# Kernel tuning notes

Measured on AMD Instinct MI355X. Metric: run time of the kernel, lower is better.

## Reference

```python
import jax, jax.numpy as jnp
import numpy as np
from jax import lax

E = 16          # num_experts
CAP = 256       # capacity
MAX_IT = 3      # max_iterations
LPF = 2.0       # load_penalty_factor
DTEMP = 2.0     # diversity_temp
MIN_USAGE = 0.05
NC = 10         # num_classes
TC = 256        # trunk_channels
B = 2048
MIN_TOK = max(1, int(B * MIN_USAGE))        # 102
K_STATIC = min(B, max(CAP, MIN_TOK))        # static top-k width per expert claim


def setup_inputs() -> dict:
    key = jax.random.key(0)
    ks = jax.random.split(key, 16)
    d = {}
    d['x'] = jax.random.normal(ks[0], (B, 3, 32, 32), jnp.float32)
    chans = [(3, 32), (32, 64), (64, 128), (128, 256)]
    for i, (ci, co) in enumerate(chans, 1):
        d[f'cw{i}'] = jax.random.normal(ks[i], (co, ci, 3, 3), jnp.float32) * (1.0 / np.sqrt(ci * 9))
        d[f'cb{i}'] = jnp.zeros((co,), jnp.float32)
        d[f'g{i}'] = jnp.ones((co,), jnp.float32)
        d[f'be{i}'] = jnp.zeros((co,), jnp.float32)
        d[f'm{i}'] = jnp.zeros((co,), jnp.float32)
        d[f'v{i}'] = jnp.ones((co,), jnp.float32)
    d['gw1'] = jax.random.normal(ks[5], (E, TC, TC // 2), jnp.float32) * 0.05
    d['gb1'] = jnp.zeros((E, TC // 2), jnp.float32)
    d['gw2'] = jax.random.normal(ks[6], (E, TC // 2), jnp.float32) * 0.05
    d['gb2'] = jnp.zeros((E,), jnp.float32)
    d['cls_w'] = jax.random.normal(ks[7], (E, NC, TC), jnp.float32) * 0.01
    d['cls_b'] = jnp.zeros((E, NC), jnp.float32)
    d['usage_ema'] = jnp.ones((E,), jnp.float32) / E
    return d


def _conv_bn_relu(x, w, b, g, beta, m, v):
    y = lax.conv_general_dilated(x, w, (1, 1), 'SAME', dimension_numbers=('NCHW', 'OIHW', 'NCHW'))
    y = y + b[None, :, None, None]
    scale = (g / jnp.sqrt(v + 1e-5))[None, :, None, None]
    return jax.nn.relu((y - m[None, :, None, None]) * scale + beta[None, :, None, None])


def _maxpool2(x):
    return lax.reduce_window(x, -jnp.inf, lax.max, (1, 1, 2, 2), (1, 1, 2, 2), 'VALID')


def _forward(x, cw1, cb1, g1, be1, m1, v1, cw2, cb2, g2, be2, m2, v2,
             cw3, cb3, g3, be3, m3, v3, cw4, cb4, g4, be4, m4, v4,
             gw1, gb1, gw2, gb2, cls_w, cls_b, usage_ema):
    # trunk (eval-mode BN)
    h = _conv_bn_relu(x, cw1, cb1, g1, be1, m1, v1)
    h = _conv_bn_relu(h, cw2, cb2, g2, be2, m2, v2)
    h = _maxpool2(h)
    h = _conv_bn_relu(h, cw3, cb3, g3, be3, m3, v3)
    h = _conv_bn_relu(h, cw4, cb4, g4, be4, m4, v4)
    h = _maxpool2(h)
    feats = h.mean(axis=(2, 3))  # AdaptiveAvgPool2d(1)+Flatten -> [B, TC]

    # per-expert classifier heads
    logits_e = jnp.einsum('bd,ecd->bec', feats, cls_w) + cls_b[None]  # [B,E,NC]
    probs = jax.nn.softmax(logits_e, axis=2)
    ent = -(probs * jnp.log(jnp.clip(probs, 1e-12))).sum(axis=2)      # [B,E]
    confidence = -ent

    # per-expert gates (vectorized over experts); dropout is identity in eval
    hidden = jax.nn.relu(jnp.einsum('bd,edh->beh', feats, gw1) + gb1[None])
    expert_scores = (jnp.einsum('beh,eh->be', hidden, gw2) + gb2[None]) / DTEMP

    routing_scores = 0.6 * expert_scores + 0.4 * confidence - LPF * usage_ema[None]

    # iterative capacity-constrained routing (eval: expert order 0..E-1)
    D = jnp.zeros((B, E), bool)
    loads = jnp.zeros((E,), jnp.float32)
    avail = jnp.ones((B,), bool)
    ranks = jnp.arange(K_STATIC)
    for it in range(MAX_IT):
        # penalty from loads at the START of the iteration
        pscores = routing_scores - (it + 1) * LPF * loads[None]
        for j in range(E):
            sj = jnp.where(avail, pscores[:, j], -jnp.inf)
            vc = avail.sum().astype(jnp.int32)
            rc = jnp.maximum(0, CAP - loads[j].astype(jnp.int32))
            ntc = jnp.where((rc == 0) | (vc == 0), 0,
                            jnp.maximum(jnp.minimum(rc, vc), jnp.minimum(MIN_TOK, vc)))
            _, idx = lax.top_k(sj, K_STATIC)
            take = ranks < ntc
            claimed = jnp.zeros((B,), bool).at[idx].set(take)
            D = D.at[:, j].set(D[:, j] | claimed)
            avail = avail & ~claimed
            loads = loads.at[j].add(ntc.astype(jnp.float32))

    # fallback: sequentially assign leftover tokens to least-loaded of top-3
    def fb(carry, inp):
        Dc, lc = carry
        sc, av, i = inp
        _, t3 = lax.top_k(sc, 3)
        best = t3[jnp.argmin(lc[t3])]
        Dc = Dc.at[i, best].set(Dc[i, best] | av)
        lc = lc.at[best].add(av.astype(jnp.float32))
        return (Dc, lc), None

    (D, loads), _ = lax.scan(fb, (D, loads), (routing_scores, avail, jnp.arange(B)))

    Df = D.astype(jnp.float32)
    active = routing_scores * Df
    active = active - active.max(axis=1, keepdims=True)
    weights = jax.nn.softmax(active + (Df - 1.0) * 1e9, axis=1)
    final_logits = (weights[:, :, None] * logits_e).sum(axis=1)
    return final_logits, routing_scores, D


def reference(x, cw1, cb1, g1, be1, m1, v1, cw2, cb2, g2, be2, m2, v2,
              cw3, cb3, g3, be3, m3, v3, cw4, cb4, g4, be4, m4, v4,
              gw1, gb1, gw2, gb2, cls_w, cls_b, usage_ema):
    return _forward(x, cw1, cb1, g1, be1, m1, v1, cw2, cb2, g2, be2, m2, v2,
                    cw3, cb3, g3, be3, m3, v3, cw4, cb4, g4, be4, m4, v4,
                    gw1, gb1, gw2, gb2, cls_w, cls_b, usage_ema)
```

## Files before the change

### kernel.cpp

```cpp
#include <hip/hip_runtime.h>

typedef __attribute__((ext_vector_type(8))) short short8;
typedef __attribute__((ext_vector_type(4))) float f32x4;

__device__ __forceinline__ unsigned short f2bf(float f) {
  unsigned u = __float_as_uint(f);
  unsigned r = (u + 0x7fffu + ((u >> 16) & 1u)) >> 16;
  return (unsigned short)r;
}
__device__ __forceinline__ float bf2f(unsigned short h) {
  return __uint_as_float(((unsigned)h) << 16);
}

__global__ __launch_bounds__(256) void bnprep_kernel(
    const float* __restrict__ g, const float* __restrict__ be,
    const float* __restrict__ m, const float* __restrict__ v,
    const float* __restrict__ b, float* __restrict__ A, float* __restrict__ C, int n)
{
  int i = blockIdx.x * 256 + threadIdx.x;
  if (i < n) {
    float s = g[i] / sqrtf(v[i] + 1e-5f);
    A[i] = s;
    C[i] = (b[i] - m[i]) * s + be[i];
  }
}

__global__ __launch_bounds__(256) void wprep2_kernel(
    const float* __restrict__ w, unsigned short* __restrict__ wPk, int CO, int CI)
{
  int NCB = CI / 32, NF = CO / 16;
  int total = 9 * NCB * NF * 64;
  int idx = blockIdx.x * 256 + threadIdx.x;
  if (idx >= total) return;
  int lane = idx & 63;
  int unit = idx >> 6;
  int f = unit % NF;
  int cb = (unit / NF) % NCB;
  int s = unit / (NF * NCB);
  int co = f * 16 + (lane & 15);
  int ci0 = cb * 32 + (lane >> 4) * 8;
  long base = (long)unit * 1024 + lane * 8;
  #pragma unroll
  for (int j = 0; j < 8; ++j) {
    float v = w[((long)co * CI + ci0 + j) * 9 + s];
    unsigned short h = f2bf(v);
    unsigned short l = f2bf(v - bf2f(h));
    wPk[base + j] = h;
    wPk[base + 512 + j] = l;
  }
}

__global__ __launch_bounds__(512, 2) void conv12_kernel(
    const float* __restrict__ xin, const float* __restrict__ cw1,
    const float* __restrict__ A1p, const float* __restrict__ C1p,
    const unsigned short* __restrict__ wPk, const float* __restrict__ Ap,
    const float* __restrict__ Cp, unsigned short* __restrict__ outA)
{
  constexpr int TY = 16, TX = 32;
  constexpr int PXW = TX + 2;
  constexpr int PXT = (TY + 2) * PXW;
  constexpr int PLSTR = PXT * 8 + 8;
  constexpr int NF = 4;
  __shared__ alignas(16) unsigned short smem[8 * PLSTR];
  __shared__ alignas(16) float sx[2160];
  __shared__ alignas(16) float sw[864];

  const int nwg = gridDim.x;
  const int orig = blockIdx.x;
  const int q = nwg >> 3, r = nwg & 7;
  const int xcd = orig & 7, pos = orig >> 3;
  const int bx = (xcd < r ? xcd * (q + 1) : r * (q + 1) + (xcd - r) * q) + pos;

  const int img = bx >> 1;
  const int tY0 = (bx & 1) * 16;

  const int tid = threadIdx.x;
  const int lane = tid & 63;
  const int lx = lane & 15, kg = lane >> 4;
  const int w = tid >> 6;

  for (int i = tid; i < 2160; i += 512) {
    int c = i / 720, rem = i - c * 720;
    int yy = rem / 36, xx2 = rem - yy * 36;
    int gy = tY0 + yy - 2, gx = xx2 - 2;
    sx[i] = (gy >= 0 && gy < 32 && gx >= 0 && gx < 32)
            ? xin[(long)img * 3072 + c * 1024 + gy * 32 + gx] : 0.f;
  }
  for (int i = tid; i < 864; i += 512) {
    int co = i & 31, kk = i >> 5;
    sw[kk * 32 + co] = cw1[(long)co * 27 + kk];
  }
  __syncthreads();

  #pragma unroll 1
  for (int p = 0; p < 2; ++p) {
    int px = p * 512 + tid;
    if (px < PXT) {
      int ry = px / PXW, rx = px - ry * PXW;
      int gy = tY0 + ry - 1, gx = rx - 1;
      if (gy >= 0 && gy < 32 && gx >= 0 && gx < 32) {
        #pragma unroll 1
        for (int half = 0; half < 2; ++half) {
          float acc[16];
          #pragma unroll
          for (int j = 0; j < 16; ++j) acc[j] = 0.f;
          #pragma unroll
          for (int c = 0; c < 3; ++c) {
            #pragma unroll
            for (int k = 0; k < 9; ++k) {
              int dy = k / 3, dx = k - 3 * (k / 3);
              float iv = sx[c * 720 + (ry + dy) * 36 + rx + dx];
              const float4* w4 = (const float4*)(sw + (c * 9 + k) * 32 + half * 16);
              #pragma unroll
              for (int q2 = 0; q2 < 4; ++q2) {
                float4 wv = w4[q2];
                acc[4 * q2 + 0] += iv * wv.x; acc[4 * q2 + 1] += iv * wv.y;
                acc[4 * q2 + 2] += iv * wv.z; acc[4 * q2 + 3] += iv * wv.w;
              }
            }
          }
          #pragma unroll
          for (int j2 = 0; j2 < 2; ++j2) {
            short8 hv, lv;
            #pragma unroll
            for (int j = 0; j < 8; ++j) {
              int co = half * 16 + j2 * 8 + j;
              float vv = fmaxf(acc[j2 * 8 + j] * A1p[co] + C1p[co], 0.f);
              unsigned short h = f2bf(vv);
              hv[j] = (short)h;
              lv[j] = (short)f2bf(vv - bf2f(h));
            }
            int plane = half * 2 + j2;
            *(short8*)(smem + plane * PLSTR + px * 8) = hv;
            *(short8*)(smem + (plane + 4) * PLSTR + px * 8) = lv;
          }
        }
      } else {
        short8 zz = {0, 0, 0, 0, 0, 0, 0, 0};
        #pragma unroll
        for (int cc = 0; cc < 8; ++cc)
          *(short8*)(smem + cc * PLSTR + px * 8) = zz;
      }
    }
  }
  __syncthreads();

  f32x4 acc[4][4];
  #pragma unroll
  for (int i = 0; i < 4; ++i)
    #pragma unroll
    for (int j = 0; j < 4; ++j) acc[i][j] = (f32x4){0.f, 0.f, 0.f, 0.f};

  for (int s = 0; s < 9; ++s) {
    const int ky = s / 3, kx = s - 3 * (s / 3);
    const long ub = ((long)(s * NF)) * 1024 + lane * 8;
    short8 bh[4], bl[4];
    #pragma unroll
    for (int nf = 0; nf < 4; ++nf) {
      bh[nf] = *(const short8*)(wPk + ub + nf * 1024);
      bl[nf] = *(const short8*)(wPk + ub + nf * 1024 + 512);
    }
    #pragma unroll
    for (int mf = 0; mf < 4; ++mf) {
      const int yoff = mf >> 1;
      const int xb = (mf & 1) * 16;
      const int y = w * 2 + yoff;
      const int pxa = (y + ky) * PXW + xb + kx + lx;
      short8 ah = *(const short8*)(smem + kg * PLSTR + pxa * 8);
      short8 al = *(const short8*)(smem + (kg + 4) * PLSTR + pxa * 8);
      #pragma unroll
      for (int nf = 0; nf < 4; ++nf)
        acc[mf][nf] = __builtin_amdgcn_mfma_f32_16x16x32_bf16(ah, bh[nf], acc[mf][nf], 0, 0, 0);
      #pragma unroll
      for (int nf = 0; nf < 4; ++nf)
        acc[mf][nf] = __builtin_amdgcn_mfma_f32_16x16x32_bf16(ah, bl[nf], acc[mf][nf], 0, 0, 0);
      #pragma unroll
      for (int nf = 0; nf < 4; ++nf)
        acc[mf][nf] = __builtin_amdgcn_mfma_f32_16x16x32_bf16(al, bh[nf], acc[mf][nf], 0, 0, 0);
    }
  }
  __syncthreads();

  float Ar[4], Cr[4];
  #pragma unroll
  for (int nf = 0; nf < 4; ++nf) {
    int co = nf * 16 + lx;
    Ar[nf] = Ap[co]; Cr[nf] = Cp[co];
  }

  unsigned short* slice = smem + w * 2048;
  const int py = (tY0 >> 1) + w;
  #pragma unroll
  for (int xf = 0; xf < 2; ++xf) {
    #pragma unroll
    for (int rp = 0; rp < 2; ++rp) {
      int ox = xf * 8 + 2 * kg + rp;
      #pragma unroll
      for (int nf = 0; nf < 4; ++nf) {
        float v0 = fmaxf(fmaxf(acc[xf][nf][2 * rp], acc[xf][nf][2 * rp + 1]),
                         fmaxf(acc[xf + 2][nf][2 * rp], acc[xf + 2][nf][2 * rp + 1]));
        float vv = fmaxf(v0 * Ar[nf] + Cr[nf], 0.f);
        unsigned short h = f2bf(vv);
        unsigned short l = f2bf(vv - bf2f(h));
        slice[(ox * 2 + 0) * 64 + nf * 16 + lx] = h;
        slice[(ox * 2 + 1) * 64 + nf * 16 + lx] = l;
      }
    }
  }
  #pragma unroll
  for (int v = 0; v < 4; ++v) {
    int hoff = lane * 8 + v * 512;
    int x2 = hoff >> 7, rem = hoff & 127;
    int seg = rem >> 6, inner = rem & 63;
    short8 d = *(const short8*)(slice + hoff);
    *(short8*)(outA + ((long)img * 256 + py * 16 + x2) * 128 + seg * 64 + inner) = d;
  }
}

__global__ __launch_bounds__(512, 1) void convmf45_kernel(
    const unsigned short* __restrict__ act2,
    const unsigned short* __restrict__ wPk3, const float* __restrict__ A3p,
    const float* __restrict__ C3p,
    const unsigned short* __restrict__ wPk4, const float* __restrict__ A4p,
    const float* __restrict__ C4p, float* __restrict__ feats)
{
  constexpr int PLSTR3 = 2056;
  constexpr int ZOFF = 32 * PLSTR3;
  constexpr int PXW2 = 18, PXT2 = 324;
  constexpr int PLSTR2 = PXT2 * 8 + 8;
  __shared__ alignas(16) unsigned short smem[ZOFF + 64];

  const int nwg = gridDim.x;
  const int orig = blockIdx.x;
  const int q = nwg >> 3, r = nwg & 7;
  const int xcd = orig & 7, pos = orig >> 3;
  const int img = (xcd < r ? xcd * (q + 1) : r * (q + 1) + (xcd - r) * q) + pos;

  const int tid = threadIdx.x;
  const int lane = tid & 63;
  const int lx = lane & 15, kg = lane >> 4;
  const int w = tid >> 6;

  if (tid < 8) {
    short8 zz = {0, 0, 0, 0, 0, 0, 0, 0};
    *(short8*)(smem + ZOFF + tid * 8) = zz;
  }

  f32x4 acc3[2][8];
  #pragma unroll
  for (int i = 0; i < 2; ++i)
    #pragma unroll
    for (int j = 0; j < 8; ++j) acc3[i][j] = (f32x4){0.f, 0.f, 0.f, 0.f};

  for (int cb = 0; cb < 2; ++cb) {
    __syncthreads();
    for (int t2 = tid; t2 < PXT2 * 8; t2 += 512) {
      int px = t2 >> 3, c = t2 & 7;
      int ry = px / PXW2, rx = px - ry * PXW2;
      int gy = ry - 1, gx = rx - 1;
      float4 v = (float4){0.f, 0.f, 0.f, 0.f};
      if (gy >= 0 && gy < 16 && gx >= 0 && gx < 16) {
        int coff = (c < 4) ? (cb * 32 + c * 8) : (64 + cb * 32 + (c - 4) * 8);
        v = *(const float4*)(act2 + ((long)img * 256 + gy * 16 + gx) * 128 + coff);
      }
      *(float4*)(smem + c * PLSTR2 + px * 8) = v;
    }
    __syncthreads();

    for (int s = 0; s < 9; ++s) {
      const int ky = s / 3, kx = s - 3 * (s / 3);
      short8 ah[2], al[2];
      #pragma unroll
      for (int mf = 0; mf < 2; ++mf) {
        const int pxa = (w * 2 + mf + ky) * PXW2 + kx + lx;
        ah[mf] = *(const short8*)(smem + kg * PLSTR2 + pxa * 8);
        al[mf] = *(const short8*)(smem + (kg + 4) * PLSTR2 + pxa * 8);
      }
      const long ub = ((long)(s * 2 + cb) * 8) * 1024 + lane * 8;
      {
        short8 bh[4], bl[4];
        #pragma unroll
        for (int nf = 0; nf < 4; ++nf) {
          bh[nf] = *(const short8*)(wPk3 + ub + nf * 1024);
          bl[nf] = *(const short8*)(wPk3 + ub + nf * 1024 + 512);
        }
        #pragma unroll
        for (int mf = 0; mf < 2; ++mf) {
          #pragma unroll
          for (int nf = 0; nf < 4; ++nf)
            acc3[mf][nf] = __builtin_amdgcn_mfma_f32_16x16x32_bf16(ah[mf], bh[nf], acc3[mf][nf], 0, 0, 0);
          #pragma unroll
          for (int nf = 0; nf < 4; ++nf)
            acc3[mf][nf] = __builtin_amdgcn_mfma_f32_16x16x32_bf16(ah[mf], bl[nf], acc3[mf][nf], 0, 0, 0);
          #pragma unroll
          for (int nf = 0; nf < 4; ++nf)
            acc3[mf][nf] = __builtin_amdgcn_mfma_f32_16x16x32_bf16(al[mf], bh[nf], acc3[mf][nf], 0, 0, 0);
        }
      }
      {
        short8 bh[4], bl[4];
        #pragma unroll
        for (int nf = 0; nf < 4; ++nf) {
          bh[nf] = *(const short8*)(wPk3 + ub + (4 + nf) * 1024);
          bl[nf] = *(const short8*)(wPk3 + ub + (4 + nf) * 1024 + 512);
        }
        #pragma unroll
        for (int mf = 0; mf < 2; ++mf) {
          #pragma unroll
          for (int nf = 0; nf < 4; ++nf)
            acc3[mf][4 + nf] = __builtin_amdgcn_mfma_f32_16x16x32_bf16(ah[mf], bh[nf], acc3[mf][4 + nf], 0, 0, 0);
          #pragma unroll
          for (int nf = 0; nf < 4; ++nf)
            acc3[mf][4 + nf] = __builtin_amdgcn_mfma_f32_16x16x32_bf16(ah[mf], bl[nf], acc3[mf][4 + nf], 0, 0, 0);
          #pragma unroll
          for (int nf = 0; nf < 4; ++nf)
            acc3[mf][4 + nf] = __builtin_amdgcn_mfma_f32_16x16x32_bf16(al[mf], bh[nf], acc3[mf][4 + nf], 0, 0, 0);
        }
      }
    }
  }
  __syncthreads();

  #pragma unroll
  for (int mf = 0; mf < 2; ++mf) {
    int y = w * 2 + mf;
    #pragma unroll
    for (int rr = 0; rr < 4; ++rr) {
      int px = y * 16 + 4 * kg + rr;
      #pragma unroll
      for (int nf = 0; nf < 8; ++nf) {
        int co = nf * 16 + lx;
        float vv = fmaxf(acc3[mf][nf][rr] * A3p[co] + C3p[co], 0.f);
        unsigned short h = f2bf(vv);
        unsigned short l = f2bf(vv - bf2f(h));
        int plane = co >> 3, j = co & 7;
        smem[plane * PLSTR3 + px * 8 + j] = h;
        smem[(plane + 16) * PLSTR3 + px * 8 + j] = l;
      }
    }
  }
  __syncthreads();

  const int pxg = w >> 1;
  const int cog = w & 1;

  f32x4 acc[4][8];
  #pragma unroll
  for (int i = 0; i < 4; ++i)
    #pragma unroll
    for (int j = 0; j < 8; ++j) acc[i][j] = (f32x4){0.f, 0.f, 0.f, 0.f};

  for (int cb = 0; cb < 4; ++cb) {
    for (int s = 0; s < 9; ++s) {
      const int ky = s / 3, kx = s - 3 * (s / 3);
      short8 ah[4], al[4];
      #pragma unroll
      for (int mf = 0; mf < 4; ++mf) {
        int gy = pxg * 4 + mf + ky - 1;
        int gxx = lx + kx - 1;
        bool ok = (gy >= 0) && (gy < 16) && (gxx >= 0) && (gxx < 16);
        int pxo = (gy * 16 + gxx) * 8;
        int offH = ok ? ((cb * 4 + kg) * PLSTR3 + pxo) : ZOFF;
        int offL = ok ? ((16 + cb * 4 + kg) * PLSTR3 + pxo) : ZOFF;
        ah[mf] = *(const short8*)(smem + offH);
        al[mf] = *(const short8*)(smem + offL);
      }
      const long ub = ((long)(s * 4 + cb) * 16 + cog * 8) * 1024 + lane * 8;
      {
        short8 bh[4], bl[4];
        #pragma unroll
        for (int nf = 0; nf < 4; ++nf) {
          bh[nf] = *(const short8*)(wPk4 + ub + nf * 1024);
          bl[nf] = *(const short8*)(wPk4 + ub + nf * 1024 + 512);
        }
        #pragma unroll
        for (int mf = 0; mf < 4; ++mf) {
          #pragma unroll
          for (int nf = 0; nf < 4; ++nf)
            acc[mf][nf] = __builtin_amdgcn_mfma_f32_16x16x32_bf16(ah[mf], bh[nf], acc[mf][nf], 0, 0, 0);
          #pragma unroll
          for (int nf = 0; nf < 4; ++nf)
            acc[mf][nf] = __builtin_amdgcn_mfma_f32_16x16x32_bf16(ah[mf], bl[nf], acc[mf][nf], 0, 0, 0);
          #pragma unroll
          for (int nf = 0; nf < 4; ++nf)
            acc[mf][nf] = __builtin_amdgcn_mfma_f32_16x16x32_bf16(al[mf], bh[nf], acc[mf][nf], 0, 0, 0);
        }
      }
      {
        short8 bh[4], bl[4];
        #pragma unroll
        for (int nf = 0; nf < 4; ++nf) {
          bh[nf] = *(const short8*)(wPk4 + ub + (4 + nf) * 1024);
          bl[nf] = *(const short8*)(wPk4 + ub + (4 + nf) * 1024 + 512);
        }
        #pragma unroll
        for (int mf = 0; mf < 4; ++mf) {
          #pragma unroll
          for (int nf = 0; nf < 4; ++nf)
            acc[mf][4 + nf] = __builtin_amdgcn_mfma_f32_16x16x32_bf16(ah[mf], bh[nf], acc[mf][4 + nf], 0, 0, 0);
          #pragma unroll
          for (int nf = 0; nf < 4; ++nf)
            acc[mf][4 + nf] = __builtin_amdgcn_mfma_f32_16x16x32_bf16(ah[mf], bl[nf], acc[mf][4 + nf], 0, 0, 0);
          #pragma unroll
          for (int nf = 0; nf < 4; ++nf)
            acc[mf][4 + nf] = __builtin_amdgcn_mfma_f32_16x16x32_bf16(al[mf], bh[nf], acc[mf][4 + nf], 0, 0, 0);
        }
      }
    }
  }
  __syncthreads();

  float psum[8];
  #pragma unroll
  for (int j = 0; j < 8; ++j) psum[j] = 0.f;
  #pragma unroll
  for (int j = 0; j < 8; ++j) {
    int co = (cog * 8 + j) * 16 + lx;
    float Ar = A4p[co], Cr = C4p[co];
    #pragma unroll
    for (int u = 0; u < 2; ++u) {
      #pragma unroll
      for (int v = 0; v < 2; ++v) {
        float vm = fmaxf(fmaxf(acc[2 * u][j][2 * v], acc[2 * u][j][2 * v + 1]),
                         fmaxf(acc[2 * u + 1][j][2 * v], acc[2 * u + 1][j][2 * v + 1]));
        psum[j] += fmaxf(vm * Ar + Cr, 0.f);
      }
    }
  }
  #pragma unroll
  for (int j = 0; j < 8; ++j) {
    psum[j] += __shfl_xor(psum[j], 16);
    psum[j] += __shfl_xor(psum[j], 32);
  }
  float* sR = (float*)smem;
  if (kg == 0) {
    #pragma unroll
    for (int j = 0; j < 8; ++j) sR[w * 128 + j * 16 + lx] = psum[j];
  }
  __syncthreads();
  if (tid < 256) {
    int cogT = tid >> 7, cl = tid & 127;
    float s = 0.f;
    #pragma unroll
    for (int p = 0; p < 4; ++p) s += sR[(p * 2 + cogT) * 128 + cl];
    feats[(long)img * 256 + tid] = s * (1.f / 64.f);
  }
}

__global__ __launch_bounds__(256) void heads2_kernel(
    const float* __restrict__ feats, const float* __restrict__ gw1,
    const float* __restrict__ gb1, const float* __restrict__ gw2,
    const float* __restrict__ gb2, const float* __restrict__ clsw,
    const float* __restrict__ clsb, const float* __restrict__ usage,
    float* __restrict__ logits_e, float* __restrict__ rs_out)
{
  __shared__ float sF[64 * 257];
  __shared__ float sLg[4 * 64 * 10];
  __shared__ float sRed[4 * 64];
  const int tid = threadIdx.x;
  const int b0 = blockIdx.x * 64;
  const int e  = blockIdx.y;

  for (int idx = tid; idx < 64 * 64; idx += 256) {
    int t = idx >> 6, dg = idx & 63;
    float4 v = ((const float4*)(feats + (long)(b0 + t) * 256))[dg];
    float* p = sF + t * 257 + dg * 4;
    p[0] = v.x; p[1] = v.y; p[2] = v.z; p[3] = v.w;
  }
  __syncthreads();

  const int t  = tid & 63;
  const int hw = __builtin_amdgcn_readfirstlane(tid >> 6);

  {
    float acc[10];
    #pragma unroll
    for (int c = 0; c < 10; ++c) acc[c] = 0.f;
    const float* fp = sF + t * 257 + hw * 64;
    const float* cw = clsw + (long)e * 2560 + hw * 64;
    for (int dd = 0; dd < 64; ++dd) {
      float f = fp[dd];
      #pragma unroll
      for (int c = 0; c < 10; ++c) acc[c] += f * cw[c * 256 + dd];
    }
    #pragma unroll
    for (int c = 0; c < 10; ++c) sLg[(hw * 64 + t) * 10 + c] = acc[c];
  }
  {
    float gacc[32];
    #pragma unroll
    for (int j = 0; j < 32; ++j) gacc[j] = 0.f;
    const float* wb = gw1 + ((long)e * 256) * 128 + hw * 32;
    const float* fp = sF + t * 257;
    for (int d = 0; d < 256; ++d) {
      float f = fp[d];
      const float4* w4 = (const float4*)(wb + (long)d * 128);
      #pragma unroll
      for (int qq = 0; qq < 8; ++qq) {
        float4 wv = w4[qq];
        gacc[4 * qq + 0] += f * wv.x; gacc[4 * qq + 1] += f * wv.y;
        gacc[4 * qq + 2] += f * wv.z; gacc[4 * qq + 3] += f * wv.w;
      }
    }
    float s = 0.f;
    const float* b1 = gb1 + e * 128 + hw * 32;
    const float* w2 = gw2 + e * 128 + hw * 32;
    #pragma unroll
    for (int j = 0; j < 32; ++j) s += fmaxf(gacc[j] + b1[j], 0.f) * w2[j];
    sRed[hw * 64 + t] = s;
  }
  __syncthreads();

  if (tid < 64) {
    float es = (sRed[t] + sRed[64 + t] + sRed[128 + t] + sRed[192 + t] + gb2[e]) * 0.5f;
    float lg[10];
    #pragma unroll
    for (int c = 0; c < 10; ++c)
      lg[c] = sLg[t * 10 + c] + sLg[(64 + t) * 10 + c]
            + sLg[(128 + t) * 10 + c] + sLg[(192 + t) * 10 + c] + clsb[e * 10 + c];
    float mx = lg[0];
    #pragma unroll
    for (int c = 1; c < 10; ++c) mx = fmaxf(mx, lg[c]);
    float S = 0.f, ps[10];
    #pragma unroll
    for (int c = 0; c < 10; ++c) { ps[c] = expf(lg[c] - mx); S += ps[c]; }
    float inv = 1.f / S, ent = 0.f;
    #pragma unroll
    for (int c = 0; c < 10; ++c) { float p = ps[c] * inv; ent -= p * logf(fmaxf(p, 1e-12f)); }
    float rsv = 0.6f * es + 0.4f * (-ent) - 2.0f * usage[e];
    rs_out[(long)(b0 + t) * 16 + e] = rsv;
    #pragma unroll
    for (int c = 0; c < 10; ++c)
      logits_e[((long)(b0 + t) * 16 + e) * 10 + c] = lg[c];
  }
}

__global__ __launch_bounds__(1024) void sort_kernel(
    const float* __restrict__ rs, unsigned* __restrict__ sortedIdx)
{
  __shared__ unsigned long long sk[2048];
  const int e = blockIdx.x;
  const unsigned tid = threadIdx.x;
  for (int i = tid; i < 2048; i += 1024) {
    float f = rs[(long)i * 16 + e];
    unsigned u = __float_as_uint(f);
    u ^= (u >> 31) ? 0xFFFFFFFFu : 0x80000000u;
    sk[i] = ((unsigned long long)(~u) << 32) | (unsigned)i;
  }
  for (unsigned k = 2; k <= 2048; k <<= 1) {
    for (unsigned j = k >> 1; j > 0; j >>= 1) {
      __syncthreads();
      unsigned i = ((tid & ~(j - 1)) << 1) | (tid & (j - 1));
      unsigned p = i | j;
      bool asc = ((i & k) == 0);
      unsigned long long a = sk[i], b = sk[p];
      if ((a > b) == asc) { sk[i] = b; sk[p] = a; }
    }
  }
  __syncthreads();
  for (int i = tid; i < 2048; i += 1024)
    sortedIdx[(long)e * 2048 + i] = (unsigned)(sk[i] & 0xFFFFFFFFull);
}

__global__ __launch_bounds__(64) void routing2_kernel(
    const unsigned* __restrict__ sortedIdx, const float* __restrict__ rs,
    unsigned* __restrict__ dmaskOut)
{
  __shared__ unsigned char sAvail[2048];
  __shared__ unsigned sDm[2048];
  __shared__ int sLoads[16];
  const int lane = threadIdx.x;
  for (int i = lane; i < 2048; i += 64) { sAvail[i] = 1; sDm[i] = 0; }
  if (lane < 16) sLoads[lane] = 0;
  __syncthreads();

  int vc = 2048;
  for (int it = 0; it < 3; ++it) {
    for (int j = 0; j < 16; ++j) {
      int lj = sLoads[j];
      int rc = 256 - lj; if (rc < 0) rc = 0;
      int ntc = 0;
      if (rc > 0 && vc > 0) {
        int a = rc < vc ? rc : vc;
        int b2 = vc < 102 ? vc : 102;
        ntc = a > b2 ? a : b2;
      }
      if (ntc > 0) {
        const unsigned* se = sortedIdx + (long)j * 2048;
        int taken = 0;
        for (int base = 0; base < 2048; base += 64) {
          if (taken >= ntc) break;
          unsigned tok = se[base + lane];
          int fl = sAvail[tok] ? 1 : 0;
          unsigned long long bm = __ballot(fl);
          int pre = taken + __popcll(bm & ((1ull << lane) - 1ull));
          if (fl && pre < ntc) { sAvail[tok] = 0; sDm[tok] |= (1u << j); }
          taken += (int)__popcll(bm);
          __syncthreads();
        }
        if (lane == 0) sLoads[j] = lj + ntc;
        vc -= ntc;
        __syncthreads();
      }
    }
  }

  if (vc > 0) {
    if (lane == 0) {
      for (int i = 0; i < 2048; ++i) {
        if (!sAvail[i]) continue;
        float s0 = -3.4e38f, s1 = s0, s2 = s0; int e0 = 0, e1 = 0, e2 = 0;
        for (int e = 0; e < 16; ++e) {
          float s = rs[i * 16 + e];
          if (s > s0)      { s2 = s1; e2 = e1; s1 = s0; e1 = e0; s0 = s; e0 = e; }
          else if (s > s1) { s2 = s1; e2 = e1; s1 = s;  e1 = e; }
          else if (s > s2) { s2 = s;  e2 = e; }
        }
        int best = e0, bl = sLoads[e0];
        if (sLoads[e1] < bl) { best = e1; bl = sLoads[e1]; }
        if (sLoads[e2] < bl) { best = e2; bl = sLoads[e2]; }
        sDm[i] |= (1u << best);
        sLoads[best] += 1;
      }
    }
    __syncthreads();
  }

  for (int i = lane; i < 2048; i += 64) dmaskOut[i] = sDm[i];
}

__global__ __launch_bounds__(256) void combine_kernel(
    const unsigned* __restrict__ dmask, const float* __restrict__ rs,
    const float* __restrict__ L, float* __restrict__ out, float* __restrict__ Dout)
{
  int i = blockIdx.x * 256 + threadIdx.x;
  if (i >= 2048) return;
  unsigned dm = dmask[i];
  float r[16];
  #pragma unroll
  for (int e = 0; e < 16; ++e) r[e] = rs[i * 16 + e];
  float mx = -3.4e38f;
  #pragma unroll
  for (int e = 0; e < 16; ++e) {
    float v = ((dm >> e) & 1u) ? r[e] : 0.0f;
    mx = fmaxf(mx, v);
  }
  float w[16], S = 0.f;
  #pragma unroll
  for (int e = 0; e < 16; ++e) {
    w[e] = ((dm >> e) & 1u) ? expf(r[e] - mx) : 0.0f;
    S += w[e];
  }
  float inv = 1.f / S;
  #pragma unroll
  for (int c = 0; c < 10; ++c) {
    float a = 0.f;
    #pragma unroll
    for (int e = 0; e < 16; ++e) a += w[e] * L[((long)i * 16 + e) * 10 + c];
    out[i * 10 + c] = a * inv;
  }
  #pragma unroll
  for (int e = 0; e < 16; ++e)
    Dout[(long)i * 16 + e] = ((dm >> e) & 1u) ? 1.0f : 0.0f;
}

extern "C" void kernel_launch(void* const* d_in, const int* in_sizes, int n_in,
                              void* d_out, int out_size, void* d_ws, size_t ws_size,
                              hipStream_t stream)
{
  const float* x    = (const float*)d_in[0];
  const float* cw1  = (const float*)d_in[1];
  const float* cb1  = (const float*)d_in[2];
  const float* g1   = (const float*)d_in[3];
  const float* be1  = (const float*)d_in[4];
  const float* m1   = (const float*)d_in[5];
  const float* v1   = (const float*)d_in[6];
  const float* cw2  = (const float*)d_in[7];
  const float* cb2  = (const float*)d_in[8];
  const float* g2   = (const float*)d_in[9];
  const float* be2  = (const float*)d_in[10];
  const float* m2   = (const float*)d_in[11];
  const float* v2   = (const float*)d_in[12];
  const float* cw3  = (const float*)d_in[13];
  const float* cb3  = (const float*)d_in[14];
  const float* g3   = (const float*)d_in[15];
  const float* be3  = (const float*)d_in[16];
  const float* m3   = (const float*)d_in[17];
  const float* v3   = (const float*)d_in[18];
  const float* cw4  = (const float*)d_in[19];
  const float* cb4  = (const float*)d_in[20];
  const float* g4   = (const float*)d_in[21];
  const float* be4  = (const float*)d_in[22];
  const float* m4   = (const float*)d_in[23];
  const float* v4   = (const float*)d_in[24];
  const float* gw1  = (const float*)d_in[25];
  const float* gb1  = (const float*)d_in[26];
  const float* gw2  = (const float*)d_in[27];
  const float* gb2  = (const float*)d_in[28];
  const float* clsw = (const float*)d_in[29];
  const float* clsb = (const float*)d_in[30];
  const float* usage = (const float*)d_in[31];

  float* out = (float*)d_out;
  float* ws  = (float*)d_ws;

  float* A1 = ws + 0;   float* C1 = ws + 32;
  float* A2 = ws + 64;  float* C2 = ws + 128;
  float* A3 = ws + 192; float* C3 = ws + 320;
  float* A4 = ws + 448; float* C4 = ws + 704;
  float* feats   = ws + 1024;
  float* logitsE = ws + 525312;
  unsigned* sortedIdx = (unsigned*)(ws + 852992);
  unsigned* dmask     = (unsigned*)(ws + 885760);
  unsigned short* wPk2 = (unsigned short*)(ws + 887808);
  unsigned short* wPk3 = (unsigned short*)(ws + 906240);
  unsigned short* wPk4 = (unsigned short*)(ws + 979968);
  const long bufBase = 1274880;

  long wsFloats = (long)(ws_size / 4);
  long availF = wsFloats - bufBase;
  long chunkL = availF / 16384;
  int chunk = (int)(chunkL < 1 ? 1 : (chunkL > 2048 ? 2048 : chunkL));

  bnprep_kernel<<<1, 256, 0, stream>>>(g1, be1, m1, v1, cb1, A1, C1, 32);
  bnprep_kernel<<<1, 256, 0, stream>>>(g2, be2, m2, v2, cb2, A2, C2, 64);
  bnprep_kernel<<<1, 256, 0, stream>>>(g3, be3, m3, v3, cb3, A3, C3, 128);
  bnprep_kernel<<<1, 256, 0, stream>>>(g4, be4, m4, v4, cb4, A4, C4, 256);
  wprep2_kernel<<<(2304 + 255) / 256, 256, 0, stream>>>(cw2, wPk2, 64, 32);
  wprep2_kernel<<<(9216 + 255) / 256, 256, 0, stream>>>(cw3, wPk3, 128, 64);
  wprep2_kernel<<<(36864 + 255) / 256, 256, 0, stream>>>(cw4, wPk4, 256, 128);

  unsigned short* act2buf = (unsigned short*)(ws + bufBase);

  for (int ib = 0; ib < 2048; ib += chunk) {
    int n = 2048 - ib; if (n > chunk) n = chunk;
    conv12_kernel<<<dim3(n * 2), 512, 0, stream>>>(
        x + (long)ib * 3072, cw1, A1, C1, wPk2, A2, C2, act2buf);
    convmf45_kernel<<<dim3(n), 512, 0, stream>>>(
        act2buf, wPk3, A3, C3, wPk4, A4, C4, feats + (long)ib * 256);
  }

  float* rsOut = out + 20480;
  heads2_kernel<<<dim3(32, 16), 256, 0, stream>>>(feats, gw1, gb1, gw2, gb2,
                                                  clsw, clsb, usage, logitsE, rsOut);
  sort_kernel<<<16, 1024, 0, stream>>>(rsOut, sortedIdx);
  routing2_kernel<<<1, 64, 0, stream>>>(sortedIdx, rsOut, dmask);
  combine_kernel<<<8, 256, 0, stream>>>(dmask, rsOut, logitsE, out, out + 53248);
}
```

Before: 1.212 ms.

## Fuse conv1-2 into the conv3-4 trunk kernel, keeping act2 in LDS

Merges the conv12 and convmf45 kernels into one per-image trunk kernel. The two row-halves of conv1/conv2 are computed in sequence, and the pooled act2 goes straight into shared memory instead of a global buffer. This removes the act2 round trip through global memory and the chunked launch loop. The conv4 weight loads are also software-pipelined by prefetching the next step's first half. In exchange, the conv1/conv2 stage now runs at one 512-thread block per image with large LDS use (~156KB) and occupancy 1, where it used to run two blocks per image at occupancy 2, so latency hiding may drop.

```diff
diff --git a/kernel.cpp b/kernel.cpp
--- a/kernel.cpp
+++ b/kernel.cpp
@@ -50,185 +50,23 @@
   }
 }
 
-__global__ __launch_bounds__(512, 2) void conv12_kernel(
+__global__ __launch_bounds__(512, 1) void trunk_kernel(
     const float* __restrict__ xin, const float* __restrict__ cw1,
     const float* __restrict__ A1p, const float* __restrict__ C1p,
-    const unsigned short* __restrict__ wPk, const float* __restrict__ Ap,
-    const float* __restrict__ Cp, unsigned short* __restrict__ outA)
-{
-  constexpr int TY = 16, TX = 32;
-  constexpr int PXW = TX + 2;
-  constexpr int PXT = (TY + 2) * PXW;
-  constexpr int PLSTR = PXT * 8 + 8;
-  constexpr int NF = 4;
-  __shared__ alignas(16) unsigned short smem[8 * PLSTR];
-  __shared__ alignas(16) float sx[2160];
-  __shared__ alignas(16) float sw[864];
-
-  const int nwg = gridDim.x;
-  const int orig = blockIdx.x;
-  const int q = nwg >> 3, r = nwg & 7;
-  const int xcd = orig & 7, pos = orig >> 3;
-  const int bx = (xcd < r ? xcd * (q + 1) : r * (q + 1) + (xcd - r) * q) + pos;
-
-  const int img = bx >> 1;
-  const int tY0 = (bx & 1) * 16;
-
-  const int tid = threadIdx.x;
-  const int lane = tid & 63;
-  const int lx = lane & 15, kg = lane >> 4;
-  const int w = tid >> 6;
-
-  for (int i = tid; i < 2160; i += 512) {
-    int c = i / 720, rem = i - c * 720;
-    int yy = rem / 36, xx2 = rem - yy * 36;
-    int gy = tY0 + yy - 2, gx = xx2 - 2;
-    sx[i] = (gy >= 0 && gy < 32 && gx >= 0 && gx < 32)
-            ? xin[(long)img * 3072 + c * 1024 + gy * 32 + gx] : 0.f;
-  }
-  for (int i = tid; i < 864; i += 512) {
-    int co = i & 31, kk = i >> 5;
-    sw[kk * 32 + co] = cw1[(long)co * 27 + kk];
-  }
-  __syncthreads();
-
-  #pragma unroll 1
-  for (int p = 0; p < 2; ++p) {
-    int px = p * 512 + tid;
-    if (px < PXT) {
-      int ry = px / PXW, rx = px - ry * PXW;
-      int gy = tY0 + ry - 1, gx = rx - 1;
-      if (gy >= 0 && gy < 32 && gx >= 0 && gx < 32) {
-        #pragma unroll 1
-        for (int half = 0; half < 2; ++half) {
-          float acc[16];
-          #pragma unroll
-          for (int j = 0; j < 16; ++j) acc[j] = 0.f;
-          #pragma unroll
-          for (int c = 0; c < 3; ++c) {
-            #pragma unroll
-            for (int k = 0; k < 9; ++k) {
-              int dy = k / 3, dx = k - 3 * (k / 3);
-              float iv = sx[c * 720 + (ry + dy) * 36 + rx + dx];
-              const float4* w4 = (const float4*)(sw + (c * 9 + k) * 32 + half * 16);
-              #pragma unroll
-              for (int q2 = 0; q2 < 4; ++q2) {
-                float4 wv = w4[q2];
-                acc[4 * q2 + 0] += iv * wv.x; acc[4 * q2 + 1] += iv * wv.y;
-                acc[4 * q2 + 2] += iv * wv.z; acc[4 * q2 + 3] += iv * wv.w;
-              }
-            }
-          }
-          #pragma unroll
-          for (int j2 = 0; j2 < 2; ++j2) {
-            short8 hv, lv;
-            #pragma unroll
-            for (int j = 0; j < 8; ++j) {
-              int co = half * 16 + j2 * 8 + j;
-              float vv = fmaxf(acc[j2 * 8 + j] * A1p[co] + C1p[co], 0.f);
-              unsigned short h = f2bf(vv);
-              hv[j] = (short)h;
-              lv[j] = (short)f2bf(vv - bf2f(h));
-            }
-            int plane = half * 2 + j2;
-            *(short8*)(smem + plane * PLSTR + px * 8) = hv;
-            *(short8*)(smem + (plane + 4) * PLSTR + px * 8) = lv;
-          }
-        }
-      } else {
-        short8 zz = {0, 0, 0, 0, 0, 0, 0, 0};
-        #pragma unroll
-        for (int cc = 0; cc < 8; ++cc)
-          *(short8*)(smem + cc * PLSTR + px * 8) = zz;
-      }
-    }
-  }
-  __syncthreads();
-
-  f32x4 acc[4][4];
-  #pragma unroll
-  for (int i = 0; i < 4; ++i)
-    #pragma unroll
-    for (int j = 0; j < 4; ++j) acc[i][j] = (f32x4){0.f, 0.f, 0.f, 0.f};
-
-  for (int s = 0; s < 9; ++s) {
-    const int ky = s / 3, kx = s - 3 * (s / 3);
-    const long ub = ((long)(s * NF)) * 1024 + lane * 8;
-    short8 bh[4], bl[4];
-    #pragma unroll
-    for (int nf = 0; nf < 4; ++nf) {
-      bh[nf] = *(const short8*)(wPk + ub + nf * 1024);
-      bl[nf] = *(const short8*)(wPk + ub + nf * 1024 + 512);
-    }
-    #pragma unroll
-    for (int mf = 0; mf < 4; ++mf) {
-      const int yoff = mf >> 1;
-      const int xb = (mf & 1) * 16;
-      const int y = w * 2 + yoff;
-      const int pxa = (y + ky) * PXW + xb + kx + lx;
-      short8 ah = *(const short8*)(smem + kg * PLSTR + pxa * 8);
-      short8 al = *(const short8*)(smem + (kg + 4) * PLSTR + pxa * 8);
-      #pragma unroll
-      for (int nf = 0; nf < 4; ++nf)
-        acc[mf][nf] = __builtin_amdgcn_mfma_f32_16x16x32_bf16(ah, bh[nf], acc[mf][nf], 0, 0, 0);
-      #pragma unroll
-      for (int nf = 0; nf < 4; ++nf)
-        acc[mf][nf] = __builtin_amdgcn_mfma_f32_16x16x32_bf16(ah, bl[nf], acc[mf][nf], 0, 0, 0);
-      #pragma unroll
-      for (int nf = 0; nf < 4; ++nf)
-        acc[mf][nf] = __builtin_amdgcn_mfma_f32_16x16x32_bf16(al, bh[nf], acc[mf][nf], 0, 0, 0);
-    }
-  }
-  __syncthreads();
-
-  float Ar[4], Cr[4];
-  #pragma unroll
-  for (int nf = 0; nf < 4; ++nf) {
-    int co = nf * 16 + lx;
-    Ar[nf] = Ap[co]; Cr[nf] = Cp[co];
-  }
-
-  unsigned short* slice = smem + w * 2048;
-  const int py = (tY0 >> 1) + w;
-  #pragma unroll
-  for (int xf = 0; xf < 2; ++xf) {
-    #pragma unroll
-    for (int rp = 0; rp < 2; ++rp) {
-      int ox = xf * 8 + 2 * kg + rp;
-      #pragma unroll
-      for (int nf = 0; nf < 4; ++nf) {
-        float v0 = fmaxf(fmaxf(acc[xf][nf][2 * rp], acc[xf][nf][2 * rp + 1]),
-                         fmaxf(acc[xf + 2][nf][2 * rp], acc[xf + 2][nf][2 * rp + 1]));
-        float vv = fmaxf(v0 * Ar[nf] + Cr[nf], 0.f);
-        unsigned short h = f2bf(vv);
-        unsigned short l = f2bf(vv - bf2f(h));
-        slice[(ox * 2 + 0) * 64 + nf * 16 + lx] = h;
-        slice[(ox * 2 + 1) * 64 + nf * 16 + lx] = l;
-      }
-    }
-  }
-  #pragma unroll
-  for (int v = 0; v < 4; ++v) {
-    int hoff = lane * 8 + v * 512;
-    int x2 = hoff >> 7, rem = hoff & 127;
-    int seg = rem >> 6, inner = rem & 63;
-    short8 d = *(const short8*)(slice + hoff);
-    *(short8*)(outA + ((long)img * 256 + py * 16 + x2) * 128 + seg * 64 + inner) = d;
-  }
-}
-
-__global__ __launch_bounds__(512, 1) void convmf45_kernel(
-    const unsigned short* __restrict__ act2,
+    const unsigned short* __restrict__ wPk2, const float* __restrict__ A2p,
+    const float* __restrict__ C2p,
     const unsigned short* __restrict__ wPk3, const float* __restrict__ A3p,
     const float* __restrict__ C3p,
     const unsigned short* __restrict__ wPk4, const float* __restrict__ A4p,
     const float* __restrict__ C4p, float* __restrict__ feats)
 {
-  constexpr int PLSTR3 = 2056;
-  constexpr int ZOFF = 32 * PLSTR3;
-  constexpr int PXW2 = 18, PXT2 = 324;
-  constexpr int PLSTR2 = PXT2 * 8 + 8;
-  __shared__ alignas(16) unsigned short smem[ZOFF + 64];
+  constexpr int OFF_A1 = 6048;
+  constexpr int PL1 = 4904;
+  constexpr int OFF_A2 = 45280;
+  constexpr int PL2 = 2056;
+  constexpr int ZOFF = 78176;
+  constexpr int PXW = 34, PXT = 612;
+  __shared__ alignas(16) unsigned short smem[78240];
 
   const int nwg = gridDim.x;
   const int orig = blockIdx.x;
@@ -241,10 +79,142 @@
   const int lx = lane & 15, kg = lane >> 4;
   const int w = tid >> 6;
 
+  float* sxf = (float*)smem;
+
   if (tid < 8) {
     short8 zz = {0, 0, 0, 0, 0, 0, 0, 0};
     *(short8*)(smem + ZOFF + tid * 8) = zz;
   }
+  for (int i = tid; i < 864; i += 512) {
+    int co = i & 31, kk = i >> 5;
+    sxf[2160 + kk * 32 + co] = cw1[(long)co * 27 + kk];
+  }
+
+  #pragma unroll 1
+  for (int t = 0; t < 2; ++t) {
+    const int tY0 = t * 16;
+    __syncthreads();
+    for (int i = tid; i < 2160; i += 512) {
+      int c = i / 720, rem = i - c * 720;
+      int yy = rem / 36, xx2 = rem - yy * 36;
+      int gy = tY0 + yy - 2, gx = xx2 - 2;
+      sxf[i] = (gy >= 0 && gy < 32 && gx >= 0 && gx < 32)
+               ? xin[(long)img * 3072 + c * 1024 + gy * 32 + gx] : 0.f;
+    }
+    __syncthreads();
+
+    #pragma unroll 1
+    for (int p = 0; p < 2; ++p) {
+      int px = p * 512 + tid;
+      if (px < PXT) {
+        int ry = px / PXW, rx = px - ry * PXW;
+        int gy = tY0 + ry - 1, gx = rx - 1;
+        if (gy >= 0 && gy < 32 && gx >= 0 && gx < 32) {
+          #pragma unroll 1
+          for (int half = 0; half < 2; ++half) {
+            float acc[16];
+            #pragma unroll
+            for (int j = 0; j < 16; ++j) acc[j] = 0.f;
+            #pragma unroll
+            for (int c = 0; c < 3; ++c) {
+              #pragma unroll
+              for (int k = 0; k < 9; ++k) {
+                int dy = k / 3, dx = k - 3 * (k / 3);
+                float iv = sxf[c * 720 + (ry + dy) * 36 + rx + dx];
+                const float4* w4 = (const float4*)(sxf + 2160 + (c * 9 + k) * 32 + half * 16);
+                #pragma unroll
+                for (int q2 = 0; q2 < 4; ++q2) {
+                  float4 wv = w4[q2];
+                  acc[4 * q2 + 0] += iv * wv.x; acc[4 * q2 + 1] += iv * wv.y;
+                  acc[4 * q2 + 2] += iv * wv.z; acc[4 * q2 + 3] += iv * wv.w;
+                }
+              }
+            }
+            #pragma unroll
+            for (int j2 = 0; j2 < 2; ++j2) {
+              short8 hv, lv;
+              #pragma unroll
+              for (int j = 0; j < 8; ++j) {
+                int co = half * 16 + j2 * 8 + j;
+                float vv = fmaxf(acc[j2 * 8 + j] * A1p[co] + C1p[co], 0.f);
+                unsigned short h = f2bf(vv);
+                hv[j] = (short)h;
+                lv[j] = (short)f2bf(vv - bf2f(h));
+              }
+              int plane = half * 2 + j2;
+              *(short8*)(smem + OFF_A1 + plane * PL1 + px * 8) = hv;
+              *(short8*)(smem + OFF_A1 + (plane + 4) * PL1 + px * 8) = lv;
+            }
+          }
+        } else {
+          short8 zz = {0, 0, 0, 0, 0, 0, 0, 0};
+          #pragma unroll
+          for (int cc = 0; cc < 8; ++cc)
+            *(short8*)(smem + OFF_A1 + cc * PL1 + px * 8) = zz;
+        }
+      }
+    }
+    __syncthreads();
+
+    f32x4 acc[4][4];
+    #pragma unroll
+    for (int i = 0; i < 4; ++i)
+      #pragma unroll
+      for (int j = 0; j < 4; ++j) acc[i][j] = (f32x4){0.f, 0.f, 0.f, 0.f};
+
+    for (int s = 0; s < 9; ++s) {
+      const int ky = s / 3, kx = s - 3 * (s / 3);
+      const long ub = ((long)(s * 4)) * 1024 + lane * 8;
+      short8 bh[4], bl[4];
+      #pragma unroll
+      for (int nf = 0; nf < 4; ++nf) {
+        bh[nf] = *(const short8*)(wPk2 + ub + nf * 1024);
+        bl[nf] = *(const short8*)(wPk2 + ub + nf * 1024 + 512);
+      }
+      #pragma unroll
+      for (int mf = 0; mf < 4; ++mf) {
+        const int yoff = mf >> 1;
+        const int xb = (mf & 1) * 16;
+        const int y = w * 2 + yoff;
+        const int pxa = (y + ky) * PXW + xb + kx + lx;
+        short8 ah = *(const short8*)(smem + OFF_A1 + kg * PL1 + pxa * 8);
+        short8 al = *(const short8*)(smem + OFF_A1 + (kg + 4) * PL1 + pxa * 8);
+        #pragma unroll
+        for (int nf = 0; nf < 4; ++nf)
+          acc[mf][nf] = __builtin_amdgcn_mfma_f32_16x16x32_bf16(ah, bh[nf], acc[mf][nf], 0, 0, 0);
+        #pragma unroll
+        for (int nf = 0; nf < 4; ++nf)
+          acc[mf][nf] = __builtin_amdgcn_mfma_f32_16x16x32_bf16(ah, bl[nf], acc[mf][nf], 0, 0, 0);
+        #pragma unroll
+        for (int nf = 0; nf < 4; ++nf)
+          acc[mf][nf] = __builtin_amdgcn_mfma_f32_16x16x32_bf16(al, bh[nf], acc[mf][nf], 0, 0, 0);
+      }
+    }
+    __syncthreads();
+
+    const int py = (tY0 >> 1) + w;
+    #pragma unroll
+    for (int xf = 0; xf < 2; ++xf) {
+      #pragma unroll
+      for (int rp = 0; rp < 2; ++rp) {
+        int ox = xf * 8 + 2 * kg + rp;
+        int px2 = py * 16 + ox;
+        #pragma unroll
+        for (int nf = 0; nf < 4; ++nf) {
+          int co = nf * 16 + lx;
+          float v0 = fmaxf(fmaxf(acc[xf][nf][2 * rp], acc[xf][nf][2 * rp + 1]),
+                           fmaxf(acc[xf + 2][nf][2 * rp], acc[xf + 2][nf][2 * rp + 1]));
+          float vv = fmaxf(v0 * A2p[co] + C2p[co], 0.f);
+          unsigned short h = f2bf(vv);
+          unsigned short l = f2bf(vv - bf2f(h));
+          int plane = co >> 3, j = co & 7;
+          smem[OFF_A2 + plane * PL2 + px2 * 8 + j] = h;
+          smem[OFF_A2 + (8 + plane) * PL2 + px2 * 8 + j] = l;
+        }
+      }
+    }
+  }
+  __syncthreads();
 
   f32x4 acc3[2][8];
   #pragma unroll
@@ -252,29 +222,22 @@
     #pragma unroll
     for (int j = 0; j < 8; ++j) acc3[i][j] = (f32x4){0.f, 0.f, 0.f, 0.f};
 
+  #pragma unroll 1
   for (int cb = 0; cb < 2; ++cb) {
-    __syncthreads();
-    for (int t2 = tid; t2 < PXT2 * 8; t2 += 512) {
-      int px = t2 >> 3, c = t2 & 7;
-      int ry = px / PXW2, rx = px - ry * PXW2;
-      int gy = ry - 1, gx = rx - 1;
-      float4 v = (float4){0.f, 0.f, 0.f, 0.f};
-      if (gy >= 0 && gy < 16 && gx >= 0 && gx < 16) {
-        int coff = (c < 4) ? (cb * 32 + c * 8) : (64 + cb * 32 + (c - 4) * 8);
-        v = *(const float4*)(act2 + ((long)img * 256 + gy * 16 + gx) * 128 + coff);
-      }
-      *(float4*)(smem + c * PLSTR2 + px * 8) = v;
-    }
-    __syncthreads();
-
+    #pragma unroll 1
     for (int s = 0; s < 9; ++s) {
       const int ky = s / 3, kx = s - 3 * (s / 3);
       short8 ah[2], al[2];
       #pragma unroll
       for (int mf = 0; mf < 2; ++mf) {
-        const int pxa = (w * 2 + mf + ky) * PXW2 + kx + lx;
-        ah[mf] = *(const short8*)(smem + kg * PLSTR2 + pxa * 8);
-        al[mf] = *(const short8*)(smem + (kg + 4) * PLSTR2 + pxa * 8);
+        int gy = w * 2 + mf + ky - 1;
+        int gxx = lx + kx - 1;
+        bool ok = (gy >= 0) && (gy < 16) && (gxx >= 0) && (gxx < 16);
+        int pxo = (gy * 16 + gxx) * 8;
+        int offH = ok ? (OFF_A2 + (cb * 4 + kg) * PL2 + pxo) : ZOFF;
+        int offL = ok ? (OFF_A2 + (8 + cb * 4 + kg) * PL2 + pxo) : ZOFF;
+        ah[mf] = *(const short8*)(smem + offH);
+        al[mf] = *(const short8*)(smem + offL);
       }
       const long ub = ((long)(s * 2 + cb) * 8) * 1024 + lane * 8;
       {
@@ -334,8 +297,8 @@
         unsigned short h = f2bf(vv);
         unsigned short l = f2bf(vv - bf2f(h));
         int plane = co >> 3, j = co & 7;
-        smem[plane * PLSTR3 + px * 8 + j] = h;
-        smem[(plane + 16) * PLSTR3 + px * 8 + j] = l;
+        smem[plane * PL2 + px * 8 + j] = h;
+        smem[(plane + 16) * PL2 + px * 8 + j] = l;
       }
     }
   }
@@ -350,60 +313,69 @@
     #pragma unroll
     for (int j = 0; j < 8; ++j) acc[i][j] = (f32x4){0.f, 0.f, 0.f, 0.f};
 
-  for (int cb = 0; cb < 4; ++cb) {
-    for (int s = 0; s < 9; ++s) {
-      const int ky = s / 3, kx = s - 3 * (s / 3);
-      short8 ah[4], al[4];
-      #pragma unroll
-      for (int mf = 0; mf < 4; ++mf) {
-        int gy = pxg * 4 + mf + ky - 1;
-        int gxx = lx + kx - 1;
-        bool ok = (gy >= 0) && (gy < 16) && (gxx >= 0) && (gxx < 16);
-        int pxo = (gy * 16 + gxx) * 8;
-        int offH = ok ? ((cb * 4 + kg) * PLSTR3 + pxo) : ZOFF;
-        int offL = ok ? ((16 + cb * 4 + kg) * PLSTR3 + pxo) : ZOFF;
-        ah[mf] = *(const short8*)(smem + offH);
-        al[mf] = *(const short8*)(smem + offL);
-      }
-      const long ub = ((long)(s * 4 + cb) * 16 + cog * 8) * 1024 + lane * 8;
-      {
-        short8 bh[4], bl[4];
+  {
+    short8 p4h[4], p4l[4];
+    long ub = ((long)cog * 8) * 1024 + lane * 8;
+    #pragma unroll
+    for (int nf = 0; nf < 4; ++nf) {
+      p4h[nf] = *(const short8*)(wPk4 + ub + nf * 1024);
+      p4l[nf] = *(const short8*)(wPk4 + ub + nf * 1024 + 512);
+    }
+    #pragma unroll 1
+    for (int cb = 0; cb < 4; ++cb) {
+      #pragma unroll 1
+      for (int s = 0; s < 9; ++s) {
+        const int ky = s / 3, kx = s - 3 * (s / 3);
+        short8 ah[4], al[4];
+        #pragma unroll
+        for (int mf = 0; mf < 4; ++mf) {
+          int gy = pxg * 4 + mf + ky - 1;
+          int gxx = lx + kx - 1;
+          bool ok = (gy >= 0) && (gy < 16) && (gxx >= 0) && (gxx < 16);
+          int pxo = (gy * 16 + gxx) * 8;
+          int offH = ok ? ((cb * 4 + kg) * PL2 + pxo) : ZOFF;
+          int offL = ok ? ((16 + cb * 4 + kg) * PL2 + pxo) : ZOFF;
+          ah[mf] = *(const short8*)(smem + offH);
+          al[mf] = *(const short8*)(smem + offL);
+        }
+        short8 c1h[4], c1l[4];
         #pragma unroll
         for (int nf = 0; nf < 4; ++nf) {
-          bh[nf] = *(const short8*)(wPk4 + ub + nf * 1024);
-          bl[nf] = *(const short8*)(wPk4 + ub + nf * 1024 + 512);
+          c1h[nf] = *(const short8*)(wPk4 + ub + (4 + nf) * 1024);
+          c1l[nf] = *(const short8*)(wPk4 + ub + (4 + nf) * 1024 + 512);
         }
         #pragma unroll
         for (int mf = 0; mf < 4; ++mf) {
           #pragma unroll
           for (int nf = 0; nf < 4; ++nf)
-            acc[mf][nf] = __builtin_amdgcn_mfma_f32_16x16x32_bf16(ah[mf], bh[nf], acc[mf][nf], 0, 0, 0);
-          #pragma unroll
-          for (int nf = 0; nf < 4; ++nf)
-            acc[mf][nf] = __builtin_amdgcn_mfma_f32_16x16x32_bf16(ah[mf], bl[nf], acc[mf][nf], 0, 0, 0);
-          #pragma unroll
-          for (int nf = 0; nf < 4; ++nf)
-            acc[mf][nf] = __builtin_amdgcn_mfma_f32_16x16x32_bf16(al[mf], bh[nf], acc[mf][nf], 0, 0, 0);
-        }
-      }
-      {
-        short8 bh[4], bl[4];
-        #pragma unroll
-        for (int nf = 0; nf < 4; ++nf) {
-          bh[nf] = *(const short8*)(wPk4 + ub + (4 + nf) * 1024);
-          bl[nf] = *(const short8*)(wPk4 + ub + (4 + nf) * 1024 + 512);
-        }
+            acc[mf][nf] = __builtin_amdgcn_mfma_f32_16x16x32_bf16(ah[mf], p4h[nf], acc[mf][nf], 0, 0, 0);
+          #pragma unroll
+          for (int nf = 0; nf < 4; ++nf)
+            acc[mf][nf] = __builtin_amdgcn_mfma_f32_16x16x32_bf16(ah[mf], p4l[nf], acc[mf][nf], 0, 0, 0);
+          #pragma unroll
+          for (int nf = 0; nf < 4; ++nf)
+            acc[mf][nf] = __builtin_amdgcn_mfma_f32_16x16x32_bf16(al[mf], p4h[nf], acc[mf][nf], 0, 0, 0);
+        }
+        long ubn = (s < 8) ? (ub + 65536) : (ub - 507904);
+        if (!(cb == 3 && s == 8)) {
+          #pragma unroll
+          for (int nf = 0; nf < 4; ++nf) {
+            p4h[nf] = *(const short8*)(wPk4 + ubn + nf * 1024);
+            p4l[nf] = *(const short8*)(wPk4 + ubn + nf * 1024 + 512);
+          }
+        }
+        ub = ubn;
         #pragma unroll
         for (int mf = 0; mf < 4; ++mf) {
           #pragma unroll
           for (int nf = 0; nf < 4; ++nf)
-            acc[mf][4 + nf] = __builtin_amdgcn_mfma_f32_16x16x32_bf16(ah[mf], bh[nf], acc[mf][4 + nf], 0, 0, 0);
-          #pragma unroll
-          for (int nf = 0; nf < 4; ++nf)
-            acc[mf][4 + nf] = __builtin_amdgcn_mfma_f32_16x16x32_bf16(ah[mf], bl[nf], acc[mf][4 + nf], 0, 0, 0);
-          #pragma unroll
-          for (int nf = 0; nf < 4; ++nf)
-            acc[mf][4 + nf] = __builtin_amdgcn_mfma_f32_16x16x32_bf16(al[mf], bh[nf], acc[mf][4 + nf], 0, 0, 0);
+            acc[mf][4 + nf] = __builtin_amdgcn_mfma_f32_16x16x32_bf16(ah[mf], c1h[nf], acc[mf][4 + nf], 0, 0, 0);
+          #pragma unroll
+          for (int nf = 0; nf < 4; ++nf)
+            acc[mf][4 + nf] = __builtin_amdgcn_mfma_f32_16x16x32_bf16(ah[mf], c1l[nf], acc[mf][4 + nf], 0, 0, 0);
+          #pragma unroll
+          for (int nf = 0; nf < 4; ++nf)
+            acc[mf][4 + nf] = __builtin_amdgcn_mfma_f32_16x16x32_bf16(al[mf], c1h[nf], acc[mf][4 + nf], 0, 0, 0);
         }
       }
     }
@@ -715,12 +687,6 @@
   unsigned short* wPk2 = (unsigned short*)(ws + 887808);
   unsigned short* wPk3 = (unsigned short*)(ws + 906240);
   unsigned short* wPk4 = (unsigned short*)(ws + 979968);
-  const long bufBase = 1274880;
-
-  long wsFloats = (long)(ws_size / 4);
-  long availF = wsFloats - bufBase;
-  long chunkL = availF / 16384;
-  int chunk = (int)(chunkL < 1 ? 1 : (chunkL > 2048 ? 2048 : chunkL));
 
   bnprep_kernel<<<1, 256, 0, stream>>>(g1, be1, m1, v1, cb1, A1, C1, 32);
   bnprep_kernel<<<1, 256, 0, stream>>>(g2, be2, m2, v2, cb2, A2, C2, 64);
@@ -730,15 +696,8 @@
   wprep2_kernel<<<(9216 + 255) / 256, 256, 0, stream>>>(cw3, wPk3, 128, 64);
   wprep2_kernel<<<(36864 + 255) / 256, 256, 0, stream>>>(cw4, wPk4, 256, 128);
 
-  unsigned short* act2buf = (unsigned short*)(ws + bufBase);
-
-  for (int ib = 0; ib < 2048; ib += chunk) {
-    int n = 2048 - ib; if (n > chunk) n = chunk;
-    conv12_kernel<<<dim3(n * 2), 512, 0, stream>>>(
-        x + (long)ib * 3072, cw1, A1, C1, wPk2, A2, C2, act2buf);
-    convmf45_kernel<<<dim3(n), 512, 0, stream>>>(
-        act2buf, wPk3, A3, C3, wPk4, A4, C4, feats + (long)ib * 256);
-  }
+  trunk_kernel<<<dim3(2048), 512, 0, stream>>>(
+      x, cw1, A1, C1, wPk2, A2, C2, wPk3, A3, C3, wPk4, A4, C4, feats);
 
   float* rsOut = out + 20480;
   heads2_kernel<<<dim3(32, 16), 256, 0, stream>>>(feats, gw1, gb1, gw2, gb2,
```

After: 1.685 ms. 1.39x slower.
